# Kernel optimization log

Hardware: AMD Instinct MI355X
Metric: run time of the kernel (lower is better)

Reference implementation:

```python
import jax, jax.numpy as jnp
import numpy as np

N = 6144      # num_nodes
E = 256       # embed_dim
H = 4         # num_heads
D = E // H    # head_dim
EPS_LN = 1e-5


def setup_inputs() -> dict:
    key = jax.random.key(0)
    ks = jax.random.split(key, 8)
    x = jax.random.normal(ks[0], (N, E), jnp.float32)
    adj = (jax.random.uniform(ks[1], (N, N)) < 0.01).astype(jnp.float32)
    adj = jnp.maximum(adj, jnp.eye(N, dtype=jnp.float32))
    s = 1.0 / np.sqrt(E)
    Wq = jax.random.normal(ks[2], (E, E), jnp.float32) * s
    Wk = jax.random.normal(ks[3], (E, E), jnp.float32) * s
    Wv = jax.random.normal(ks[4], (E, E), jnp.float32) * s
    Wo = jax.random.normal(ks[5], (E, E), jnp.float32) * s
    bq = jnp.zeros((E,), jnp.float32)
    bk = jnp.zeros((E,), jnp.float32)
    bv = jnp.zeros((E,), jnp.float32)
    bo = jnp.zeros((E,), jnp.float32)
    gamma = jnp.ones((E,), jnp.float32)
    beta = jnp.zeros((E,), jnp.float32)
    return {"embeddings": x, "adj_matrix": adj,
            "Wq": Wq, "bq": bq, "Wk": Wk, "bk": bk, "Wv": Wv, "bv": bv,
            "Wo": Wo, "bo": bo, "gamma": gamma, "beta": beta}


def reference(embeddings, adj_matrix, Wq, bq, Wk, bk, Wv, bv, Wo, bo, gamma, beta):
    n, e = embeddings.shape
    h, d = H, e // H
    # linear projections (torch nn.Linear: x @ W.T + b)
    Q = (embeddings @ Wq.T + bq).reshape(n, h, d)
    K = (embeddings @ Wk.T + bk).reshape(n, h, d)
    V = (embeddings @ Wv.T + bv).reshape(n, h, d)
    # per-head node-node attention scores [h, n, n]
    scores = jnp.einsum('nhd,mhd->hnm', Q, K) / np.sqrt(d)
    scores = jnp.where(adj_matrix[None, :, :] == 0, -jnp.inf, scores)
    attn = jax.nn.softmax(scores, axis=-1)  # [h, n, n]
    out = jnp.einsum('hnm,mhd->nhd', attn, V).reshape(n, e)
    out = out @ Wo.T + bo
    # residual + LayerNorm
    y = embeddings + out
    mu = jnp.mean(y, axis=-1, keepdims=True)
    var = jnp.var(y, axis=-1, keepdims=True)
    return (y - mu) * jax.lax.rsqrt(var + EPS_LN) * gamma + beta
```

## Files before the change

### kernel.cpp

```cpp
#include <hip/hip_runtime.h>
#include <hip/hip_fp16.h>
#include <math.h>

constexpr int kN  = 6144;
constexpr int kE  = 256;
constexpr int kD  = 64;
constexpr int CAP = 128;

typedef float    f32x4  __attribute__((ext_vector_type(4)));
typedef _Float16 half8  __attribute__((ext_vector_type(8)));

__global__ __launch_bounds__(256) void convert_h(
    const float* __restrict__ X,
    const float* __restrict__ Wq, const float* __restrict__ Wk,
    const float* __restrict__ Wv, const float* __restrict__ Wo,
    __half* __restrict__ Xh,
    __half* __restrict__ Wqh, __half* __restrict__ Wkh,
    __half* __restrict__ Wvh, __half* __restrict__ Woh)
{
    const int i = blockIdx.x * 256 + threadIdx.x;
    const float* src; __half* dst; int off;
    if      (i < 393216) { src = X;  dst = Xh;  off = i; }
    else if (i < 409600) { src = Wq; dst = Wqh; off = i - 393216; }
    else if (i < 425984) { src = Wk; dst = Wkh; off = i - 409600; }
    else if (i < 442368) { src = Wv; dst = Wvh; off = i - 425984; }
    else                 { src = Wo; dst = Woh; off = i - 442368; }
    const float4 v = ((const float4*)src)[off];
    const __half2 a = __float22half2_rn(make_float2(v.x, v.y));
    const __half2 b = __float22half2_rn(make_float2(v.z, v.w));
    ((__half2*)dst)[off * 2 + 0] = a;
    ((__half2*)dst)[off * 2 + 1] = b;
}

__device__ __forceinline__ void gemm_mfma_h(
    const __half* __restrict__ A, const __half* __restrict__ B,
    const float* __restrict__ bias, __half* __restrict__ Cout,
    const int n0, const int c0)
{
    const int lane = threadIdx.x & 63;
    const int w    = threadIdx.x >> 6;
    const int ar   = n0 + w * 16 + (lane & 15);
    const int ko   = (lane >> 4) * 8;

    f32x4 acc[4] = {{0.f,0.f,0.f,0.f},{0.f,0.f,0.f,0.f},
                    {0.f,0.f,0.f,0.f},{0.f,0.f,0.f,0.f}};

#pragma unroll
    for (int kc = 0; kc < kE; kc += 32) {
        const half8 af = *(const half8*)(A + (size_t)ar * kE + kc + ko);
#pragma unroll
        for (int j = 0; j < 4; ++j) {
            const int c = c0 + j * 16 + (lane & 15);
            const half8 bf = *(const half8*)(B + (size_t)c * kE + kc + ko);
            acc[j] = __builtin_amdgcn_mfma_f32_16x16x32_f16(af, bf, acc[j], 0, 0, 0);
        }
    }

    const int orow = n0 + w * 16 + (lane >> 4) * 4;
    const int ocol = lane & 15;
#pragma unroll
    for (int j = 0; j < 4; ++j) {
        const int c = c0 + j * 16 + ocol;
        const float bi = bias[c];
#pragma unroll
        for (int r = 0; r < 4; ++r)
            Cout[(size_t)(orow + r) * kE + c] = __float2half(acc[j][r] + bi);
    }
}

__global__ __launch_bounds__(256) void proj_csr(
    const __half* __restrict__ Xh,
    const __half* __restrict__ Wqh, const float* __restrict__ bq,
    const __half* __restrict__ Wkh, const float* __restrict__ bk,
    const __half* __restrict__ Wvh, const float* __restrict__ bv,
    __half* __restrict__ Q, __half* __restrict__ K, __half* __restrict__ V,
    const float* __restrict__ adj,
    int* __restrict__ csr_cnt, int* __restrict__ csr_col)
{
    if (blockIdx.x < kN / 4) {
        const int lane = threadIdx.x & 63;
        const int r    = blockIdx.x * 4 + (threadIdx.x >> 6);
        const float* arow = adj + (size_t)r * kN;
        int* out = csr_col + (size_t)r * CAP;
        int base = 0;
#pragma unroll 4
        for (int it = 0; it < kN / 256; ++it) {
            const int col = it * 256 + lane * 4;
            const f32x4 a = __builtin_nontemporal_load((const f32x4*)(arow + col));
            const unsigned long long m0 = __ballot(a[0] != 0.f);
            const unsigned long long m1 = __ballot(a[1] != 0.f);
            const unsigned long long m2 = __ballot(a[2] != 0.f);
            const unsigned long long m3 = __ballot(a[3] != 0.f);
            const int c0 = __popcll(m0), c1 = __popcll(m1);
            const int c2 = __popcll(m2), c3 = __popcll(m3);
            const unsigned long long below = (1ull << lane) - 1ull;
            const int p0 = __popcll(m0 & below);
            const int p1 = c0 + __popcll(m1 & below);
            const int p2 = c0 + c1 + __popcll(m2 & below);
            const int p3 = c0 + c1 + c2 + __popcll(m3 & below);
            if (a[0] != 0.f && base + p0 < CAP) out[base + p0] = col + 0;
            if (a[1] != 0.f && base + p1 < CAP) out[base + p1] = col + 1;
            if (a[2] != 0.f && base + p2 < CAP) out[base + p2] = col + 2;
            if (a[3] != 0.f && base + p3 < CAP) out[base + p3] = col + 3;
            base += c0 + c1 + c2 + c3;
        }
        if (lane == 0) csr_cnt[r] = (base < CAP) ? base : CAP;
    } else {
        const int b = blockIdx.x - kN / 4;
        const int m = b / 384;
        const int r = b % 384;
        const int n0 = (r >> 2) * 64, c0 = (r & 3) * 64;
        if (m == 0)      gemm_mfma_h(Xh, Wqh, bq, Q, n0, c0);
        else if (m == 1) gemm_mfma_h(Xh, Wkh, bk, K, n0, c0);
        else             gemm_mfma_h(Xh, Wvh, bv, V, n0, c0);
    }
}

__global__ __launch_bounds__(256) void attn_csr(
    const int* __restrict__ csr_cnt, const int* __restrict__ csr_col,
    const __half* __restrict__ Qm,
    const __half* __restrict__ Km,
    const __half* __restrict__ Vm,
    __half* __restrict__ O)
{
    const int n    = blockIdx.x;
    const int t    = threadIdx.x;
    const int lane = t & 63;
    const int head = t >> 6;

    __shared__ int   nbr[CAP];
    __shared__ float q_lds[kE];
    __shared__ float p_lds[4][64];

    const int cnt = min(csr_cnt[n], CAP);
    if (t < CAP && t < cnt) nbr[t] = csr_col[(size_t)n * CAP + t];
    q_lds[t] = __half2float(Qm[(size_t)n * kE + t]);
    __syncthreads();

    float m = -INFINITY, lsum = 0.f, oacc = 0.f;
    const __half* Vh = Vm + head * kD;

    for (int b0 = 0; b0 < cnt; b0 += 64) {
        const int  bcnt  = min(64, cnt - b0);
        const bool valid = lane < bcnt;
        const int  idx   = valid ? nbr[b0 + lane] : n;
        const float4* krow = (const float4*)(Km + (size_t)idx * kE + head * kD);

        float s = 0.f;
#pragma unroll
        for (int i = 0; i < 8; ++i) {
            const float4 raw = krow[i];
            const float2 f0 = __half22float2(*(const __half2*)&raw.x);
            const float2 f1 = __half22float2(*(const __half2*)&raw.y);
            const float2 f2 = __half22float2(*(const __half2*)&raw.z);
            const float2 f3 = __half22float2(*(const __half2*)&raw.w);
            const float* qv = &q_lds[head * kD + i * 8];
            s += f0.x * qv[0] + f0.y * qv[1] + f1.x * qv[2] + f1.y * qv[3]
               + f2.x * qv[4] + f2.y * qv[5] + f3.x * qv[6] + f3.y * qv[7];
        }
        s *= 0.125f;
        if (!valid) s = -INFINITY;

        float bmax = s;
#pragma unroll
        for (int o = 32; o >= 1; o >>= 1) bmax = fmaxf(bmax, __shfl_xor(bmax, o, 64));
        const float mnew  = fmaxf(m, bmax);
        const float scale = __expf(m - mnew);
        const float p     = valid ? __expf(s - mnew) : 0.f;
        float bsum = p;
#pragma unroll
        for (int o = 32; o >= 1; o >>= 1) bsum += __shfl_xor(bsum, o, 64);
        lsum = lsum * scale + bsum;
        m    = mnew;
        oacc *= scale;

        p_lds[head][lane] = p;
        __syncthreads();

        int l = 0;
        for (; l + 8 <= bcnt; l += 8) {
            float pv[8], vv[8];
#pragma unroll
            for (int u = 0; u < 8; ++u) {
                const int vrow = nbr[b0 + l + u];
                vv[u] = __half2float(Vh[(size_t)vrow * kE + lane]);
                pv[u] = p_lds[head][l + u];
            }
#pragma unroll
            for (int u = 0; u < 8; ++u) oacc += pv[u] * vv[u];
        }
        for (; l < bcnt; ++l)
            oacc += p_lds[head][l] * __half2float(Vh[(size_t)nbr[b0 + l] * kE + lane]);
        __syncthreads();
    }

    O[(size_t)n * kE + head * kD + lane] = __float2half(oacc / lsum);
}

__global__ __launch_bounds__(256) void oproj_ln(
    const __half* __restrict__ A, const __half* __restrict__ Woh,
    const float* __restrict__ bo, const float* __restrict__ X,
    const float* __restrict__ gamma, const float* __restrict__ beta,
    float* __restrict__ Out)
{
    const int n0   = blockIdx.x * 16;
    const int t    = threadIdx.x;
    const int lane = t & 63;
    const int w    = t >> 6;
    const int ar   = n0 + (lane & 15);
    const int ko   = (lane >> 4) * 8;

    __shared__ float sm_s[4][16], sm_q[4][16];

    f32x4 acc[4] = {{0.f,0.f,0.f,0.f},{0.f,0.f,0.f,0.f},
                    {0.f,0.f,0.f,0.f},{0.f,0.f,0.f,0.f}};

#pragma unroll
    for (int kc = 0; kc < kE; kc += 32) {
        const half8 af = *(const half8*)(A + (size_t)ar * kE + kc + ko);
#pragma unroll
        for (int j = 0; j < 4; ++j) {
            const int c = w * 64 + j * 16 + (lane & 15);
            const half8 bf = *(const half8*)(Woh + (size_t)c * kE + kc + ko);
            acc[j] = __builtin_amdgcn_mfma_f32_16x16x32_f16(af, bf, acc[j], 0, 0, 0);
        }
    }

    const int orow = n0 + (lane >> 4) * 4;
    const int ocol = lane & 15;

#pragma unroll
    for (int j = 0; j < 4; ++j) {
        const int c = w * 64 + j * 16 + ocol;
        const float bi = bo[c];
#pragma unroll
        for (int r = 0; r < 4; ++r)
            acc[j][r] += bi + X[(size_t)(orow + r) * kE + c];
    }

#pragma unroll
    for (int r = 0; r < 4; ++r) {
        float s = 0.f, q = 0.f;
#pragma unroll
        for (int j = 0; j < 4; ++j) { s += acc[j][r]; q += acc[j][r] * acc[j][r]; }
#pragma unroll
        for (int o = 8; o >= 1; o >>= 1) {
            s += __shfl_xor(s, o, 64);
            q += __shfl_xor(q, o, 64);
        }
        if (ocol == 0) {
            sm_s[w][(lane >> 4) * 4 + r] = s;
            sm_q[w][(lane >> 4) * 4 + r] = q;
        }
    }
    __syncthreads();

    float mean[4], inv[4];
#pragma unroll
    for (int r = 0; r < 4; ++r) {
        const int row16 = (lane >> 4) * 4 + r;
        const float S  = sm_s[0][row16] + sm_s[1][row16] + sm_s[2][row16] + sm_s[3][row16];
        const float Qq = sm_q[0][row16] + sm_q[1][row16] + sm_q[2][row16] + sm_q[3][row16];
        mean[r] = S * (1.f / 256.f);
        const float var = Qq * (1.f / 256.f) - mean[r] * mean[r];
        inv[r] = rsqrtf(var + 1e-5f);
    }

#pragma unroll
    for (int j = 0; j < 4; ++j) {
        const int c = w * 64 + j * 16 + ocol;
        const float g  = gamma[c];
        const float be = beta[c];
#pragma unroll
        for (int r = 0; r < 4; ++r)
            Out[(size_t)(orow + r) * kE + c] = (acc[j][r] - mean[r]) * inv[r] * g + be;
    }
}

extern "C" void kernel_launch(void* const* d_in, const int* in_sizes, int n_in,
                              void* d_out, int out_size, void* d_ws, size_t ws_size,
                              hipStream_t stream)
{
    const float* x   = (const float*)d_in[0];
    const float* adj = (const float*)d_in[1];
    const float* Wq  = (const float*)d_in[2];
    const float* bq  = (const float*)d_in[3];
    const float* Wk  = (const float*)d_in[4];
    const float* bk  = (const float*)d_in[5];
    const float* Wv  = (const float*)d_in[6];
    const float* bv  = (const float*)d_in[7];
    const float* Wo  = (const float*)d_in[8];
    const float* bo  = (const float*)d_in[9];
    const float* gam = (const float*)d_in[10];
    const float* bet = (const float*)d_in[11];

    char* p = (char*)d_ws;
    int*    csr_cnt = (int*)p;            p += (size_t)kN * 4;
    int*    csr_col = (int*)p;            p += (size_t)kN * CAP * 4;
    __half* Xh      = (__half*)p;         p += (size_t)kN * kE * 2;
    __half* Wqh     = (__half*)p;         p += (size_t)kE * kE * 2;
    __half* Wkh     = (__half*)p;         p += (size_t)kE * kE * 2;
    __half* Wvh     = (__half*)p;         p += (size_t)kE * kE * 2;
    __half* Woh     = (__half*)p;         p += (size_t)kE * kE * 2;
    __half* Q       = (__half*)p;         p += (size_t)kN * kE * 2;
    __half* K       = (__half*)p;         p += (size_t)kN * kE * 2;
    __half* V       = (__half*)p;         p += (size_t)kN * kE * 2;
    float*  Y       = (float*)d_out;

    convert_h<<<1792, 256, 0, stream>>>(x, Wq, Wk, Wv, Wo, Xh, Wqh, Wkh, Wvh, Woh);
    proj_csr<<<kN / 4 + 3 * (kN / 64) * (kE / 64), 256, 0, stream>>>(
        Xh, Wqh, bq, Wkh, bk, Wvh, bv, Q, K, V, adj, csr_cnt, csr_col);
    attn_csr<<<kN, 256, 0, stream>>>(csr_cnt, csr_col, Q, K, V, Q);
    oproj_ln<<<kN / 16, 256, 0, stream>>>(Q, Woh, bo, x, gam, bet, Y);
}
```

Baseline: 125.2 us.

## Regroup kernels so adjacency scan pairs with conversion, drop attention block barriers

The adjacency-to-CSR scan now shares a launch with the fp16 conversion instead of with the QKV projection, and the projection runs as its own kernel. The change in pairing is meant to balance the memory-bound scan against lighter work rather than the GEMM. In the attention kernel, neighbour slots past the count are padded with the node's own index, so gathers need no validity select. The block-wide barriers around the per-head probability buffer are removed, since each wave only reads the slice it wrote. The value loop is unrolled by 16 with no scalar tail; padded entries carry zero weight, so they add redundant loads but no change to the result.

```diff
diff --git a/kernel.cpp b/kernel.cpp
--- a/kernel.cpp
+++ b/kernel.cpp
@@ -10,72 +10,15 @@
 typedef float    f32x4  __attribute__((ext_vector_type(4)));
 typedef _Float16 half8  __attribute__((ext_vector_type(8)));
 
-__global__ __launch_bounds__(256) void convert_h(
+__global__ __launch_bounds__(256) void scan_convert(
+    const float* __restrict__ adj,
+    int* __restrict__ csr_cnt, int* __restrict__ csr_col,
     const float* __restrict__ X,
     const float* __restrict__ Wq, const float* __restrict__ Wk,
     const float* __restrict__ Wv, const float* __restrict__ Wo,
     __half* __restrict__ Xh,
     __half* __restrict__ Wqh, __half* __restrict__ Wkh,
     __half* __restrict__ Wvh, __half* __restrict__ Woh)
-{
-    const int i = blockIdx.x * 256 + threadIdx.x;
-    const float* src; __half* dst; int off;
-    if      (i < 393216) { src = X;  dst = Xh;  off = i; }
-    else if (i < 409600) { src = Wq; dst = Wqh; off = i - 393216; }
-    else if (i < 425984) { src = Wk; dst = Wkh; off = i - 409600; }
-    else if (i < 442368) { src = Wv; dst = Wvh; off = i - 425984; }
-    else                 { src = Wo; dst = Woh; off = i - 442368; }
-    const float4 v = ((const float4*)src)[off];
-    const __half2 a = __float22half2_rn(make_float2(v.x, v.y));
-    const __half2 b = __float22half2_rn(make_float2(v.z, v.w));
-    ((__half2*)dst)[off * 2 + 0] = a;
-    ((__half2*)dst)[off * 2 + 1] = b;
-}
-
-__device__ __forceinline__ void gemm_mfma_h(
-    const __half* __restrict__ A, const __half* __restrict__ B,
-    const float* __restrict__ bias, __half* __restrict__ Cout,
-    const int n0, const int c0)
-{
-    const int lane = threadIdx.x & 63;
-    const int w    = threadIdx.x >> 6;
-    const int ar   = n0 + w * 16 + (lane & 15);
-    const int ko   = (lane >> 4) * 8;
-
-    f32x4 acc[4] = {{0.f,0.f,0.f,0.f},{0.f,0.f,0.f,0.f},
-                    {0.f,0.f,0.f,0.f},{0.f,0.f,0.f,0.f}};
-
-#pragma unroll
-    for (int kc = 0; kc < kE; kc += 32) {
-        const half8 af = *(const half8*)(A + (size_t)ar * kE + kc + ko);
-#pragma unroll
-        for (int j = 0; j < 4; ++j) {
-            const int c = c0 + j * 16 + (lane & 15);
-            const half8 bf = *(const half8*)(B + (size_t)c * kE + kc + ko);
-            acc[j] = __builtin_amdgcn_mfma_f32_16x16x32_f16(af, bf, acc[j], 0, 0, 0);
-        }
-    }
-
-    const int orow = n0 + w * 16 + (lane >> 4) * 4;
-    const int ocol = lane & 15;
-#pragma unroll
-    for (int j = 0; j < 4; ++j) {
-        const int c = c0 + j * 16 + ocol;
-        const float bi = bias[c];
-#pragma unroll
-        for (int r = 0; r < 4; ++r)
-            Cout[(size_t)(orow + r) * kE + c] = __float2half(acc[j][r] + bi);
-    }
-}
-
-__global__ __launch_bounds__(256) void proj_csr(
-    const __half* __restrict__ Xh,
-    const __half* __restrict__ Wqh, const float* __restrict__ bq,
-    const __half* __restrict__ Wkh, const float* __restrict__ bk,
-    const __half* __restrict__ Wvh, const float* __restrict__ bv,
-    __half* __restrict__ Q, __half* __restrict__ K, __half* __restrict__ V,
-    const float* __restrict__ adj,
-    int* __restrict__ csr_cnt, int* __restrict__ csr_col)
 {
     if (blockIdx.x < kN / 4) {
         const int lane = threadIdx.x & 63;
@@ -106,14 +49,70 @@
         }
         if (lane == 0) csr_cnt[r] = (base < CAP) ? base : CAP;
     } else {
-        const int b = blockIdx.x - kN / 4;
-        const int m = b / 384;
-        const int r = b % 384;
-        const int n0 = (r >> 2) * 64, c0 = (r & 3) * 64;
-        if (m == 0)      gemm_mfma_h(Xh, Wqh, bq, Q, n0, c0);
-        else if (m == 1) gemm_mfma_h(Xh, Wkh, bk, K, n0, c0);
-        else             gemm_mfma_h(Xh, Wvh, bv, V, n0, c0);
-    }
+        const int i = (blockIdx.x - kN / 4) * 256 + threadIdx.x;
+        const float* src; __half* dst; int off;
+        if      (i < 393216) { src = X;  dst = Xh;  off = i; }
+        else if (i < 409600) { src = Wq; dst = Wqh; off = i - 393216; }
+        else if (i < 425984) { src = Wk; dst = Wkh; off = i - 409600; }
+        else if (i < 442368) { src = Wv; dst = Wvh; off = i - 425984; }
+        else                 { src = Wo; dst = Woh; off = i - 442368; }
+        const float4 v = ((const float4*)src)[off];
+        const __half2 a = __float22half2_rn(make_float2(v.x, v.y));
+        const __half2 b = __float22half2_rn(make_float2(v.z, v.w));
+        ((__half2*)dst)[off * 2 + 0] = a;
+        ((__half2*)dst)[off * 2 + 1] = b;
+    }
+}
+
+__device__ __forceinline__ void gemm_mfma_h(
+    const __half* __restrict__ A, const __half* __restrict__ B,
+    const float* __restrict__ bias, __half* __restrict__ Cout,
+    const int n0, const int c0)
+{
+    const int lane = threadIdx.x & 63;
+    const int w    = threadIdx.x >> 6;
+    const int ar   = n0 + w * 16 + (lane & 15);
+    const int ko   = (lane >> 4) * 8;
+
+    f32x4 acc[4] = {{0.f,0.f,0.f,0.f},{0.f,0.f,0.f,0.f},
+                    {0.f,0.f,0.f,0.f},{0.f,0.f,0.f,0.f}};
+
+#pragma unroll
+    for (int kc = 0; kc < kE; kc += 32) {
+        const half8 af = *(const half8*)(A + (size_t)ar * kE + kc + ko);
+#pragma unroll
+        for (int j = 0; j < 4; ++j) {
+            const int c = c0 + j * 16 + (lane & 15);
+            const half8 bf = *(const half8*)(B + (size_t)c * kE + kc + ko);
+            acc[j] = __builtin_amdgcn_mfma_f32_16x16x32_f16(af, bf, acc[j], 0, 0, 0);
+        }
+    }
+
+    const int orow = n0 + w * 16 + (lane >> 4) * 4;
+    const int ocol = lane & 15;
+#pragma unroll
+    for (int j = 0; j < 4; ++j) {
+        const int c = c0 + j * 16 + ocol;
+        const float bi = bias[c];
+#pragma unroll
+        for (int r = 0; r < 4; ++r)
+            Cout[(size_t)(orow + r) * kE + c] = __float2half(acc[j][r] + bi);
+    }
+}
+
+__global__ __launch_bounds__(256) void proj3(
+    const __half* __restrict__ Xh,
+    const __half* __restrict__ Wqh, const float* __restrict__ bq,
+    const __half* __restrict__ Wkh, const float* __restrict__ bk,
+    const __half* __restrict__ Wvh, const float* __restrict__ bv,
+    __half* __restrict__ Q, __half* __restrict__ K, __half* __restrict__ V)
+{
+    const int m = blockIdx.x / 384;
+    const int r = blockIdx.x % 384;
+    const int n0 = (r >> 2) * 64, c0 = (r & 3) * 64;
+    if (m == 0)      gemm_mfma_h(Xh, Wqh, bq, Q, n0, c0);
+    else if (m == 1) gemm_mfma_h(Xh, Wkh, bk, K, n0, c0);
+    else             gemm_mfma_h(Xh, Wvh, bv, V, n0, c0);
 }
 
 __global__ __launch_bounds__(256) void attn_csr(
@@ -133,7 +132,7 @@
     __shared__ float p_lds[4][64];
 
     const int cnt = min(csr_cnt[n], CAP);
-    if (t < CAP && t < cnt) nbr[t] = csr_col[(size_t)n * CAP + t];
+    if (t < CAP) nbr[t] = (t < cnt) ? csr_col[(size_t)n * CAP + t] : n;
     q_lds[t] = __half2float(Qm[(size_t)n * kE + t]);
     __syncthreads();
 
@@ -143,7 +142,7 @@
     for (int b0 = 0; b0 < cnt; b0 += 64) {
         const int  bcnt  = min(64, cnt - b0);
         const bool valid = lane < bcnt;
-        const int  idx   = valid ? nbr[b0 + lane] : n;
+        const int  idx   = nbr[b0 + lane];
         const float4* krow = (const float4*)(Km + (size_t)idx * kE + head * kD);
 
         float s = 0.f;
@@ -175,23 +174,18 @@
         oacc *= scale;
 
         p_lds[head][lane] = p;
-        __syncthreads();
-
-        int l = 0;
-        for (; l + 8 <= bcnt; l += 8) {
-            float pv[8], vv[8];
-#pragma unroll
-            for (int u = 0; u < 8; ++u) {
+
+        for (int l = 0; l < bcnt; l += 16) {
+            float pv[16], vv[16];
+#pragma unroll
+            for (int u = 0; u < 16; ++u) {
                 const int vrow = nbr[b0 + l + u];
                 vv[u] = __half2float(Vh[(size_t)vrow * kE + lane]);
                 pv[u] = p_lds[head][l + u];
             }
 #pragma unroll
-            for (int u = 0; u < 8; ++u) oacc += pv[u] * vv[u];
-        }
-        for (; l < bcnt; ++l)
-            oacc += p_lds[head][l] * __half2float(Vh[(size_t)nbr[b0 + l] * kE + lane]);
-        __syncthreads();
+            for (int u = 0; u < 16; ++u) oacc += pv[u] * vv[u];
+        }
     }
 
     O[(size_t)n * kE + head * kD + lane] = __float2half(oacc / lsum);
@@ -307,9 +301,9 @@
     __half* V       = (__half*)p;         p += (size_t)kN * kE * 2;
     float*  Y       = (float*)d_out;
 
-    convert_h<<<1792, 256, 0, stream>>>(x, Wq, Wk, Wv, Wo, Xh, Wqh, Wkh, Wvh, Woh);
-    proj_csr<<<kN / 4 + 3 * (kN / 64) * (kE / 64), 256, 0, stream>>>(
-        Xh, Wqh, bq, Wkh, bk, Wvh, bv, Q, K, V, adj, csr_cnt, csr_col);
+    scan_convert<<<kN / 4 + 1792, 256, 0, stream>>>(
+        adj, csr_cnt, csr_col, x, Wq, Wk, Wv, Wo, Xh, Wqh, Wkh, Wvh, Woh);
+    proj3<<<1152, 256, 0, stream>>>(Xh, Wqh, bq, Wkh, bk, Wvh, bv, Q, K, V);
     attn_csr<<<kN, 256, 0, stream>>>(csr_cnt, csr_col, Q, K, V, Q);
     oproj_ln<<<kN / 16, 256, 0, stream>>>(Q, Woh, bo, x, gam, bet, Y);
 }
```

After: 154.2 us. +23.1%, slower.
